# Performance work log

Measured on AMD Instinct MI355X. Metric: run time of the kernel, lower is better.

## Reference

```python
import jax, jax.numpy as jnp
import numpy as np

# SparseSAKEEnergyModel: 6-layer sparse SAKE GNN (hidden=64, heads=4, update=False)
# followed by per-graph segment_sum and a Dense(64)->silu->Dense(1) head.
N_NODES = 10000
N_EDGES = 100000
F_IN = 16           # raw node feature dim (embedded to H by embedding_in)
H = 64              # hidden_features
HEADS = 4           # SAKE default n_heads
COEF = H * HEADS    # n_coefficients = 256
DEPTH = 6
RBF = 50            # ExpNormalSmearing num_rbf
CUT = 5.0           # ExpNormalSmearing cutoff_upper (alpha = 5/(5-0) = 1)
NUM_SEGMENTS = 100


def setup_inputs() -> dict:
    key = jax.random.key(0)
    ks = jax.random.split(key, 20)

    def dn(k, *shape):
        # Dense kernel init ~ lecun-normal-ish: std = 1/sqrt(fan_in); fan_in = shape[-2]
        return jax.random.normal(k, shape, jnp.float32) * np.float32(1.0 / np.sqrt(shape[-2]))

    start = float(np.exp(-CUT))
    rbf_means = jnp.broadcast_to(jnp.linspace(start, 1.0, RBF).astype(jnp.float32)[None], (DEPTH, RBF))
    rbf_betas = jnp.full((DEPTH, RBF), float(((2.0 / RBF) * (1.0 - start)) ** -2), jnp.float32)

    z = lambda *s: jnp.zeros(s, jnp.float32)
    return dict(
        i=jax.random.normal(ks[0], (N_NODES, F_IN), jnp.float32),
        x=jax.random.normal(ks[1], (N_NODES, 3), jnp.float32),
        emb_in_w=dn(ks[2], F_IN, H), emb_in_b=z(H),
        edge_in_w=dn(ks[3], DEPTH, 2 * H, RBF), edge_in_b=z(DEPTH, RBF),
        rbf_means=rbf_means, rbf_betas=rbf_betas,
        edge_out_w1=dn(ks[4], DEPTH, 2 * H + RBF + 1, H), edge_out_b1=z(DEPTH, H),
        edge_out_w2=dn(ks[5], DEPTH, H, H), edge_out_b2=z(DEPTH, H),
        sem_w=dn(ks[6], DEPTH, H, HEADS), sem_b=z(DEPTH, HEADS),
        xmix_w=dn(ks[7], DEPTH, COEF, COEF),
        pn_w1=dn(ks[8], DEPTH, COEF, H), pn_b1=z(DEPTH, H),
        pn_w2=dn(ks[9], DEPTH, H, H), pn_b2=z(DEPTH, H),
        node_w1=dn(ks[10], DEPTH, H + COEF + H, H), node_b1=z(DEPTH, H),
        node_w2=dn(ks[11], DEPTH, H, H), node_b2=z(DEPTH, H),
        emb_out_w1=dn(ks[12], H, H), emb_out_b1=z(H),
        emb_out_w2=dn(ks[13], H, H), emb_out_b2=z(H),
        head_w1=dn(ks[14], H, H), head_b1=z(H),
        head_w2=dn(ks[15], H, 1), head_b2=z(1),
        edges=jax.random.randint(ks[16], (N_EDGES, 2), 0, N_NODES, jnp.int32),
        graph_segments=jnp.sort(jax.random.randint(ks[17], (N_NODES,), 0, NUM_SEGMENTS, jnp.int32)),
    )


def _segment_softmax(logits, seg, num_segments):
    m = jax.ops.segment_max(logits, seg, num_segments)
    e = jnp.exp(logits - m[seg])
    s = jax.ops.segment_sum(e, seg, num_segments)
    return e / s[seg]


def _forward(i, x, emb_in_w, emb_in_b, edge_in_w, edge_in_b, rbf_means, rbf_betas,
             edge_out_w1, edge_out_b1, edge_out_w2, edge_out_b2, sem_w, sem_b, xmix_w,
             pn_w1, pn_b1, pn_w2, pn_b2, node_w1, node_b1, node_w2, node_b2,
             emb_out_w1, emb_out_b1, emb_out_w2, emb_out_b2,
             head_w1, head_b1, head_w2, head_b2, edges, graph_segments):
    N = x.shape[0]
    dst, src = edges[:, 0], edges[:, 1]
    x_minus_xt = x[dst] - x[src]                               # (E,3)
    d = jnp.sqrt((x_minus_xt ** 2).sum(-1, keepdims=True) + 1e-10)  # (E,1)
    dirs = x_minus_xt / (d + 1e-5)                             # normalized edge directions
    rbf_base = jnp.exp(-d)                                     # ExpNormalSmearing, alpha=1, lower=0

    h = i @ emb_in_w + emb_in_b                                # embedding_in -> (N,H)
    for l in range(DEPTH):
        # --- edge model: ContinuousFilterConvolutionWithConcatenation ---
        hc = jnp.concatenate([h[dst], h[src]], -1)             # (E,2H)
        hm = hc @ edge_in_w[l] + edge_in_b[l]                  # (E,RBF)
        rbf = jnp.exp(-rbf_betas[l] * (rbf_base - rbf_means[l]) ** 2)
        he = jnp.concatenate([hc, rbf * hm, d], -1)
        he = jax.nn.silu(he @ edge_out_w1[l] + edge_out_b1[l]) @ edge_out_w2[l] + edge_out_b2[l]  # (E,H)
        # --- combined (semantic * euclidean) attention, segment-softmax over dst ---
        att_s = _segment_softmax(jax.nn.celu(he @ sem_w[l] + sem_b[l], alpha=2.0), dst, N)  # (E,HEADS)
        att_e = _segment_softmax(-d, dst, N)                   # (E,1)
        att = att_e * att_s
        att = att / jax.ops.segment_sum(att, dst, N)[dst]
        hea = (he[:, :, None] * att[:, None, :]).reshape(-1, COEF)  # (E, H*HEADS)
        # --- spatial attention ---
        coef = jnp.tanh(hea @ xmix_w[l])                       # (E,COEF)
        csum = jax.ops.segment_sum(coef[:, :, None] * dirs[:, None, :], dst, N)  # (N,COEF,3)
        cnorm = (csum ** 2).sum(-1)                            # (N,COEF)
        h_comb = jax.nn.silu(jax.nn.silu(cnorm @ pn_w1[l] + pn_b1[l]) @ pn_w2[l] + pn_b2[l])
        # --- aggregate + node update (residual) ---
        h_agg = jax.ops.segment_sum(hea, dst, N)               # (N,COEF)
        upd = jnp.concatenate([h, h_agg, h_comb], -1)
        upd = jax.nn.silu(jax.nn.silu(upd @ node_w1[l] + node_b1[l]) @ node_w2[l] + node_b2[l])
        h = h + upd
    h = jax.nn.silu(h @ emb_out_w1 + emb_out_b1) @ emb_out_w2 + emb_out_b2  # embedding_out
    y = jax.ops.segment_sum(h, graph_segments, NUM_SEGMENTS)   # per-graph readout (G,H)
    return jax.nn.silu(y @ head_w1 + head_b1) @ head_w2 + head_b2  # (G,1)


def reference(i, x, emb_in_w, emb_in_b, edge_in_w, edge_in_b, rbf_means, rbf_betas,
              edge_out_w1, edge_out_b1, edge_out_w2, edge_out_b2, sem_w, sem_b, xmix_w,
              pn_w1, pn_b1, pn_w2, pn_b2, node_w1, node_b1, node_w2, node_b2,
              emb_out_w1, emb_out_b1, emb_out_w2, emb_out_b2,
              head_w1, head_b1, head_w2, head_b2, edges, graph_segments):
    return _forward(i, x, emb_in_w, emb_in_b, edge_in_w, edge_in_b, rbf_means, rbf_betas,
                    edge_out_w1, edge_out_b1, edge_out_w2, edge_out_b2, sem_w, sem_b, xmix_w,
                    pn_w1, pn_b1, pn_w2, pn_b2, node_w1, node_b1, node_w2, node_b2,
                    emb_out_w1, emb_out_b1, emb_out_w2, emb_out_b2,
                    head_w1, head_b1, head_w2, head_b2, edges, graph_segments)
```

## Files before the change

### kernel.cpp

```cpp
#include <hip/hip_runtime.h>
#include <hip/hip_bf16.h>

constexpr int EN   = 100000;
constexpr int NN   = 10000;
constexpr int DEPTH = 6;
constexpr int NSEG = 100;
constexpr int LP   = 40;

typedef unsigned short u16;
typedef __bf16 bf16x8 __attribute__((ext_vector_type(8)));
typedef float  f32x4  __attribute__((ext_vector_type(4)));

__device__ inline float wred_max(float v){
#pragma unroll
  for (int o = 32; o > 0; o >>= 1) v = fmaxf(v, __shfl_xor(v, o, 64));
  return v;
}
__device__ inline float wred_sum(float v){
#pragma unroll
  for (int o = 32; o > 0; o >>= 1) v += __shfl_xor(v, o, 64);
  return v;
}
__device__ inline float siluf(float x){ return x / (1.f + __expf(-x)); }
__device__ inline float fast_tanh(float x){
  float e = __expf(2.f * x);
  return 1.f - 2.f / (e + 1.f);
}
__device__ inline u16 f2bf(float x){
  __hip_bfloat16 h = __float2bfloat16(x);
  return *reinterpret_cast<u16*>(&h);
}
__device__ inline float bf2f(u16 u){
  union { float f; unsigned int ui; } v; v.ui = ((unsigned int)u) << 16; return v.f;
}

__global__ __launch_bounds__(256) void count_k(const int* __restrict__ edges,
                                               int* __restrict__ counts){
  int e = blockIdx.x * 256 + threadIdx.x;
  if (e >= EN) return;
  atomicAdd(&counts[edges[2*e]], 1);
}

__global__ __launch_bounds__(256) void scan_k(const int* __restrict__ counts,
                                              int* __restrict__ offs){
  __shared__ int part[256];
  const int CH = (NN + 255) / 256;
  int t = threadIdx.x;
  int s = 0;
  for (int j = 0; j < CH; ++j){ int idx = t*CH + j; if (idx < NN) s += counts[idx]; }
  part[t] = s;
  __syncthreads();
  if (t == 0){
    int run = 0;
    for (int i = 0; i < 256; ++i){ int v = part[i]; part[i] = run; run += v; }
    offs[NN] = run;
  }
  __syncthreads();
  int run = part[t];
  for (int j = 0; j < CH; ++j){
    int idx = t*CH + j;
    if (idx < NN){ offs[idx] = run; run += counts[idx]; }
  }
}

__global__ __launch_bounds__(256) void geoscat_k(const int* __restrict__ edges,
                                                 const float* __restrict__ x,
                                                 const int* __restrict__ offs,
                                                 int* __restrict__ cursor,
                                                 int* __restrict__ edge_s,
                                                 float* __restrict__ dS,
                                                 float* __restrict__ dirsS,
                                                 float* __restrict__ rbfS){
  int e = blockIdx.x * 256 + threadIdx.x;
  if (e >= EN) return;
  int dst = edges[2*e], src = edges[2*e+1];
  float dx = x[dst*3+0] - x[src*3+0];
  float dy = x[dst*3+1] - x[src*3+1];
  float dz = x[dst*3+2] - x[src*3+2];
  float dd = sqrtf(dx*dx + dy*dy + dz*dz + 1e-10f);
  float inv = 1.f / (dd + 1e-5f);
  int pos = offs[dst] + atomicAdd(&cursor[dst], 1);
  edge_s[2*pos]   = dst;
  edge_s[2*pos+1] = src;
  dS[pos]   = dd;
  rbfS[pos] = __expf(-dd);
  dirsS[3*pos+0] = dx*inv; dirsS[3*pos+1] = dy*inv; dirsS[3*pos+2] = dz*inv;
}

__global__ __launch_bounds__(256) void h2b_k(const float* __restrict__ h,
                                             u16* __restrict__ hbf,
                                             u16* __restrict__ node_in){
  int gid = blockIdx.x * 256 + threadIdx.x;
  if (gid >= NN*64) return;
  int n = gid >> 6, ch = gid & 63;
  u16 b = f2bf(h[gid]);
  hbf[gid] = b;
  node_in[(size_t)n*384 + ch] = b;
}

__global__ void convw_k(const float* __restrict__ src, int K, int N, size_t sStride,
                        u16* __restrict__ dst, int Kpad, int Npad, size_t dStride){
  int idx = blockIdx.x * 256 + threadIdx.x;
  if (idx >= Npad*Kpad) return;
  int n = idx / Kpad, k = idx - n*Kpad;
  float v = (k < K && n < N) ? src[blockIdx.y*sStride + (size_t)k*N + n] : 0.f;
  dst[blockIdx.y*dStride + idx] = f2bf(v);
}

__global__ __launch_bounds__(256) void convx_k(const float* __restrict__ xmix,
                                               u16* __restrict__ xr){
  int idx = blockIdx.x * 256 + threadIdx.x;
  int l = blockIdx.y;
  int q  = idx & 63;
  int n  = (idx >> 6) & 255;
  int hd = idx >> 14;
  xr[(size_t)l*65536 + idx] = f2bf(xmix[(size_t)l*65536 + (size_t)(4*q + hd)*256 + n]);
}

__global__ __launch_bounds__(256) void edge_fused_k(
    const int* __restrict__ edge_s,
    const u16* __restrict__ hbf,
    const float* __restrict__ rbfS,
    const float* __restrict__ dS,
    const u16* __restrict__ Winb,
    const float* __restrict__ bin,
    const float* __restrict__ mean,
    const float* __restrict__ beta,
    const u16* __restrict__ W1b,
    const float* __restrict__ b1,
    const u16* __restrict__ W2b,
    const float* __restrict__ b2,
    const float* __restrict__ sw,
    const float* __restrict__ sb,
    u16* __restrict__ he,
    float* __restrict__ logit){
  __shared__ u16 HC[64*132];
  __shared__ u16 WA[64*132];
  __shared__ u16 T2[64*72];
  __shared__ u16 WB[64*72];
  u16* HE1 = WA;
  const int tid = threadIdx.x, lane = tid & 63, wv = tid >> 6;
  const int l15 = lane & 15, kq = (lane >> 4) * 8;
  const int rsub = (lane >> 4) << 2;
  const int e0 = blockIdx.x * 64;

#pragma unroll
  for (int i = 0; i < 4; ++i){
    int idx = tid + i*256;
    int row = idx >> 4, c = idx & 15;
    int e = min(e0 + row, EN - 1);
    int node = (c < 8) ? edge_s[2*e] : edge_s[2*e+1];
    *reinterpret_cast<uint4*>(HC + row*132 + c*8) =
        *reinterpret_cast<const uint4*>(hbf + (size_t)node*64 + (c & 7)*8);
    *reinterpret_cast<uint4*>(WA + row*132 + c*8) =
        *reinterpret_cast<const uint4*>(Winb + row*128 + c*8);
  }
  __syncthreads();

  f32x4 acc[4];
#pragma unroll
  for (int mt = 0; mt < 4; ++mt) acc[mt] = (f32x4){0.f,0.f,0.f,0.f};
#pragma unroll
  for (int kc = 0; kc < 128; kc += 32){
    bf16x8 bf = *reinterpret_cast<const bf16x8*>(WA + (wv*16 + l15)*132 + kc + kq);
#pragma unroll
    for (int mt = 0; mt < 4; ++mt){
      bf16x8 af = *reinterpret_cast<const bf16x8*>(HC + (mt*16 + l15)*132 + kc + kq);
      acc[mt] = __builtin_amdgcn_mfma_f32_16x16x32_bf16(af, bf, acc[mt], 0, 0, 0);
    }
  }
  {
    int n = wv*16 + l15;
    float bi = 0.f, mn = 0.f, bt = 0.f;
    if (n < 50){ bi = bin[n]; mn = mean[n]; bt = beta[n]; }
#pragma unroll
    for (int mt = 0; mt < 4; ++mt){
#pragma unroll
      for (int r = 0; r < 4; ++r){
        int row = mt*16 + rsub + r;
        int e = min(e0 + row, EN - 1);
        float v;
        if (n < 50){ float df = rbfS[e] - mn; v = __expf(-bt*df*df) * (acc[mt][r] + bi); }
        else if (n == 50) v = dS[e];
        else v = 0.f;
        T2[row*72 + n] = f2bf(v);
      }
    }
  }
  __syncthreads();

#pragma unroll
  for (int i = 0; i < 4; ++i){
    int idx = tid + i*256;
    int row = idx >> 4, c = idx & 15;
    *reinterpret_cast<uint4*>(WA + row*132 + c*8) =
        *reinterpret_cast<const uint4*>(W1b + row*192 + c*8);
  }
#pragma unroll
  for (int i = 0; i < 2; ++i){
    int idx = tid + i*256;
    int row = idx >> 3, cc = (idx & 7)*8;
    *reinterpret_cast<uint4*>(WB + row*72 + cc) =
        *reinterpret_cast<const uint4*>(W1b + row*192 + 128 + cc);
  }
  __syncthreads();

#pragma unroll
  for (int mt = 0; mt < 4; ++mt) acc[mt] = (f32x4){0.f,0.f,0.f,0.f};
#pragma unroll
  for (int kc = 0; kc < 128; kc += 32){
    bf16x8 bf = *reinterpret_cast<const bf16x8*>(WA + (wv*16 + l15)*132 + kc + kq);
#pragma unroll
    for (int mt = 0; mt < 4; ++mt){
      bf16x8 af = *reinterpret_cast<const bf16x8*>(HC + (mt*16 + l15)*132 + kc + kq);
      acc[mt] = __builtin_amdgcn_mfma_f32_16x16x32_bf16(af, bf, acc[mt], 0, 0, 0);
    }
  }
#pragma unroll
  for (int kc = 0; kc < 64; kc += 32){
    bf16x8 bf = *reinterpret_cast<const bf16x8*>(WB + (wv*16 + l15)*72 + kc + kq);
#pragma unroll
    for (int mt = 0; mt < 4; ++mt){
      bf16x8 af = *reinterpret_cast<const bf16x8*>(T2 + (mt*16 + l15)*72 + kc + kq);
      acc[mt] = __builtin_amdgcn_mfma_f32_16x16x32_bf16(af, bf, acc[mt], 0, 0, 0);
    }
  }
  __syncthreads();
  {
    int n = wv*16 + l15;
    float bb = b1[n];
#pragma unroll
    for (int mt = 0; mt < 4; ++mt){
#pragma unroll
      for (int r = 0; r < 4; ++r){
        int row = mt*16 + rsub + r;
        HE1[row*72 + n] = f2bf(siluf(acc[mt][r] + bb));
      }
    }
  }

#pragma unroll
  for (int i = 0; i < 2; ++i){
    int idx = tid + i*256;
    int row = idx >> 3, cc = (idx & 7)*8;
    *reinterpret_cast<uint4*>(WB + row*72 + cc) =
        *reinterpret_cast<const uint4*>(W2b + row*64 + cc);
  }
  __syncthreads();

#pragma unroll
  for (int mt = 0; mt < 4; ++mt) acc[mt] = (f32x4){0.f,0.f,0.f,0.f};
#pragma unroll
  for (int kc = 0; kc < 64; kc += 32){
    bf16x8 bf = *reinterpret_cast<const bf16x8*>(WB + (wv*16 + l15)*72 + kc + kq);
#pragma unroll
    for (int mt = 0; mt < 4; ++mt){
      bf16x8 af = *reinterpret_cast<const bf16x8*>(HE1 + (mt*16 + l15)*72 + kc + kq);
      acc[mt] = __builtin_amdgcn_mfma_f32_16x16x32_bf16(af, bf, acc[mt], 0, 0, 0);
    }
  }
  {
    int n = wv*16 + l15;
    float bb = b2[n];
#pragma unroll
    for (int mt = 0; mt < 4; ++mt){
#pragma unroll
      for (int r = 0; r < 4; ++r){
        int row = mt*16 + rsub + r;
        int e = e0 + row;
        u16 hb = f2bf(acc[mt][r] + bb);
        if (e < EN) he[(size_t)e*64 + n] = hb;
        T2[row*72 + n] = hb;
      }
    }
  }
  __syncthreads();

  {
    int er = tid >> 2, hd = tid & 3;
    float a = sb[hd];
#pragma unroll 8
    for (int k = 0; k < 64; ++k)
      a = fmaf(bf2f(T2[er*72 + k]), sw[k*4 + hd], a);
    float v = a > 0.f ? a : 2.f*(__expf(0.5f*a) - 1.f);
    int e = e0 + er;
    if (e < EN) logit[(size_t)e*4 + hd] = v;
  }
}

__global__ __launch_bounds__(256) void xmix_k(const u16* __restrict__ he,
                                              const float* __restrict__ att,
                                              const u16* __restrict__ Xr,
                                              u16* __restrict__ coef){
  __shared__ u16 B_s[128*72];
  const int tid = threadIdx.x, lane = tid & 63, wave = tid >> 6;
  const int l15 = lane & 15, kq = (lane >> 4) * 8;
  const int rsub = (lane >> 4) << 2;
  const int m0 = blockIdx.x * 128;
  const int n0 = blockIdx.y * 128;

  float a32[2][2][8];
  float4 attA[2];
#pragma unroll
  for (int h = 0; h < 2; ++h){
    int m = min(m0 + h*64 + wave*16 + l15, EN - 1);
    attA[h] = *reinterpret_cast<const float4*>(att + (size_t)m*4);
#pragma unroll
    for (int k2 = 0; k2 < 2; ++k2){
      ushort4 u0 = *reinterpret_cast<const ushort4*>(he + (size_t)m*64 + k2*32 + kq);
      ushort4 u1 = *reinterpret_cast<const ushort4*>(he + (size_t)m*64 + k2*32 + kq + 4);
      a32[h][k2][0] = bf2f(u0.x); a32[h][k2][1] = bf2f(u0.y);
      a32[h][k2][2] = bf2f(u0.z); a32[h][k2][3] = bf2f(u0.w);
      a32[h][k2][4] = bf2f(u1.x); a32[h][k2][5] = bf2f(u1.y);
      a32[h][k2][6] = bf2f(u1.z); a32[h][k2][7] = bf2f(u1.w);
    }
  }

  f32x4 acc[2][8];
#pragma unroll
  for (int h = 0; h < 2; ++h)
#pragma unroll
    for (int c = 0; c < 8; ++c) acc[h][c] = (f32x4){0.f,0.f,0.f,0.f};

  const int srow = tid >> 1;
  const int scol = (tid & 1) * 32;

#pragma unroll
  for (int hd = 0; hd < 4; ++hd){
    {
      const u16* src = Xr + ((size_t)hd*256 + n0 + srow)*64 + scol;
      u16* dst = B_s + srow*72 + scol;
      *reinterpret_cast<uint4*>(dst)      = *reinterpret_cast<const uint4*>(src);
      *reinterpret_cast<uint4*>(dst + 8)  = *reinterpret_cast<const uint4*>(src + 8);
      *reinterpret_cast<uint4*>(dst + 16) = *reinterpret_cast<const uint4*>(src + 16);
      *reinterpret_cast<uint4*>(dst + 24) = *reinterpret_cast<const uint4*>(src + 24);
    }
    __syncthreads();
    bf16x8 afs[2][2];
#pragma unroll
    for (int h = 0; h < 2; ++h){
      float a = (hd==0) ? attA[h].x : (hd==1) ? attA[h].y
              : (hd==2) ? attA[h].z : attA[h].w;
#pragma unroll
      for (int k2 = 0; k2 < 2; ++k2){
        u16 o[8];
#pragma unroll
        for (int j = 0; j < 8; ++j) o[j] = f2bf(a32[h][k2][j] * a);
        afs[h][k2] = *reinterpret_cast<bf16x8*>(o);
      }
    }
#pragma unroll
    for (int k2 = 0; k2 < 2; ++k2){
#pragma unroll
      for (int c = 0; c < 8; ++c){
        bf16x8 bf = *reinterpret_cast<const bf16x8*>(B_s + (c*16 + l15)*72 + k2*32 + kq);
        acc[0][c] = __builtin_amdgcn_mfma_f32_16x16x32_bf16(afs[0][k2], bf, acc[0][c], 0, 0, 0);
        acc[1][c] = __builtin_amdgcn_mfma_f32_16x16x32_bf16(afs[1][k2], bf, acc[1][c], 0, 0, 0);
      }
    }
    __syncthreads();
  }

#pragma unroll
  for (int h = 0; h < 2; ++h){
    const int rbase = m0 + h*64 + wave*16 + rsub;
#pragma unroll
    for (int c = 0; c < 8; ++c){
      int n = n0 + c*16 + l15;
#pragma unroll
      for (int r = 0; r < 4; ++r){
        int m = rbase + r;
        if (m < EN) coef[(size_t)m*256 + n] = f2bf(fast_tanh(acc[h][c][r]));
      }
    }
  }
}

template<int MODE>
__global__ __launch_bounds__(256) void mlp2_k(const u16* __restrict__ A, int lda, int K1,
                                              const u16* __restrict__ W1t,
                                              const float* __restrict__ b1,
                                              const u16* __restrict__ W2t,
                                              const float* __restrict__ b2,
                                              int M,
                                              u16* __restrict__ node_in,
                                              const float* __restrict__ hres,
                                              float* __restrict__ hout,
                                              u16* __restrict__ hbf){
  __shared__ u16 A_s[128*LP];
  __shared__ u16 B_s[64*LP];
  __shared__ u16 T_s[128*72];
  __shared__ u16 W2_s[64*72];
  const int tid = threadIdx.x, lane = tid & 63, wave = tid >> 6;
  const int m0 = blockIdx.x * 128;
  const int l15 = lane & 15, kq = (lane >> 4)*8;
  const int rsub = (lane >> 4) << 2;
#pragma unroll
  for (int i = 0; i < 2; ++i){
    int idx = tid + i*256;
    int row = idx >> 3, cc = (idx & 7)*8;
    *reinterpret_cast<uint4*>(W2_s + row*72 + cc) =
        *reinterpret_cast<const uint4*>(W2t + row*64 + cc);
  }
  const int srow = tid >> 1, skh = (tid & 1)*16;
  const int arow = min(m0 + srow, M - 1);
  const u16* aptr = A + (size_t)arow*lda + skh;
  const int brow = tid >> 2, bcol = (tid & 3)*8;

  f32x4 acc0[4], acc1[4];
#pragma unroll
  for (int c = 0; c < 4; ++c){ acc0[c] = (f32x4){0,0,0,0}; acc1[c] = (f32x4){0,0,0,0}; }

  for (int kc = 0; kc < K1; kc += 32){
    *reinterpret_cast<uint4*>(A_s + srow*LP + skh)     = *reinterpret_cast<const uint4*>(aptr + kc);
    *reinterpret_cast<uint4*>(A_s + srow*LP + skh + 8) = *reinterpret_cast<const uint4*>(aptr + kc + 8);
    *reinterpret_cast<uint4*>(B_s + brow*LP + bcol) =
        *reinterpret_cast<const uint4*>(W1t + (size_t)brow*K1 + kc + bcol);
    __syncthreads();
    bf16x8 af0 = *reinterpret_cast<const bf16x8*>(A_s + (wave*16 + l15)*LP + kq);
    bf16x8 af1 = *reinterpret_cast<const bf16x8*>(A_s + (64 + wave*16 + l15)*LP + kq);
#pragma unroll
    for (int c = 0; c < 4; ++c){
      bf16x8 bf = *reinterpret_cast<const bf16x8*>(B_s + (c*16 + l15)*LP + kq);
      acc0[c] = __builtin_amdgcn_mfma_f32_16x16x32_bf16(af0, bf, acc0[c], 0, 0, 0);
      acc1[c] = __builtin_amdgcn_mfma_f32_16x16x32_bf16(af1, bf, acc1[c], 0, 0, 0);
    }
    __syncthreads();
  }
#pragma unroll
  for (int h = 0; h < 2; ++h){
#pragma unroll
    for (int c = 0; c < 4; ++c){
      int n = c*16 + l15;
      float bb = b1[n];
#pragma unroll
      for (int r = 0; r < 4; ++r){
        int rowloc = h*64 + wave*16 + rsub + r;
        float a = (h == 0) ? acc0[c][r] : acc1[c][r];
        T_s[rowloc*72 + n] = f2bf(siluf(a + bb));
      }
    }
  }
  __syncthreads();
#pragma unroll
  for (int c = 0; c < 4; ++c){ acc0[c] = (f32x4){0,0,0,0}; acc1[c] = (f32x4){0,0,0,0}; }
#pragma unroll
  for (int kc = 0; kc < 64; kc += 32){
    bf16x8 af0 = *reinterpret_cast<const bf16x8*>(T_s + (wave*16 + l15)*72 + kc + kq);
    bf16x8 af1 = *reinterpret_cast<const bf16x8*>(T_s + (64 + wave*16 + l15)*72 + kc + kq);
#pragma unroll
    for (int c = 0; c < 4; ++c){
      bf16x8 bf = *reinterpret_cast<const bf16x8*>(W2_s + (c*16 + l15)*72 + kc + kq);
      acc0[c] = __builtin_amdgcn_mfma_f32_16x16x32_bf16(af0, bf, acc0[c], 0, 0, 0);
      acc1[c] = __builtin_amdgcn_mfma_f32_16x16x32_bf16(af1, bf, acc1[c], 0, 0, 0);
    }
  }
#pragma unroll
  for (int h = 0; h < 2; ++h){
#pragma unroll
    for (int c = 0; c < 4; ++c){
      int n = c*16 + l15;
      float bb = b2[n];
#pragma unroll
      for (int r = 0; r < 4; ++r){
        int m = m0 + h*64 + wave*16 + rsub + r;
        if (m >= M) continue;
        float a = (h == 0) ? acc0[c][r] : acc1[c][r];
        float v = siluf(a + bb);
        if (MODE == 0){
          node_in[(size_t)m*384 + 320 + n] = f2bf(v);
        } else {
          float hn = hres[(size_t)m*64 + n] + v;
          hout[(size_t)m*64 + n] = hn;
          u16 bbf = f2bf(hn);
          hbf[(size_t)m*64 + n] = bbf;
          node_in[(size_t)m*384 + n] = bbf;
        }
      }
    }
  }
}

template<int EPI>
__global__ __launch_bounds__(256) void gemm_k(const float* __restrict__ A, int lda,
                                              const float* __restrict__ W, int ldw,
                                              const float* __restrict__ bias,
                                              float* __restrict__ out, int ldo, int ocol,
                                              int M, int N, int K){
  __shared__ float w_s[128*64];
  const int tid  = threadIdx.x;
  const int nl   = tid & 63;
  const int rg   = tid >> 6;
  const int col0 = blockIdx.y * 64;
  const int m0   = blockIdx.x * 16 + rg * 4;
  float acc[4] = {0.f, 0.f, 0.f, 0.f};
  const float* ar[4];
#pragma unroll
  for (int r = 0; r < 4; ++r){
    int mr = min(m0 + r, M - 1);
    ar[r] = A + (size_t)mr * lda;
  }
  for (int kc = 0; kc < K; kc += 128){
    int kn = min(128, K - kc);
    for (int idx = tid; idx < 128*64; idx += 256){
      int kk = idx >> 6, nn = idx & 63;
      int gn = col0 + nn;
      w_s[idx] = (kk < kn && gn < N) ? W[(size_t)(kc+kk)*ldw + gn] : 0.f;
    }
    __syncthreads();
    for (int k = 0; k < kn; ++k){
      float wv = w_s[k*64 + nl];
#pragma unroll
      for (int r = 0; r < 4; ++r) acc[r] = fmaf(ar[r][kc + k], wv, acc[r]);
    }
    __syncthreads();
  }
  int n = col0 + nl;
  if (n >= N) return;
  float b = bias ? bias[n] : 0.f;
#pragma unroll
  for (int r = 0; r < 4; ++r){
    int m = m0 + r;
    if (m >= M) break;
    float a = acc[r] + b;
    out[(size_t)m*ldo + ocol + n] = (EPI == 1) ? siluf(a) : a;
  }
}

__global__ __launch_bounds__(256) void att_k(const int* __restrict__ offs,
                                             const float* __restrict__ dS,
                                             const float* __restrict__ logit,
                                             float* __restrict__ att){
  int lane = threadIdx.x & 63;
  int node = (blockIdx.x * 256 + threadIdx.x) >> 6;
  if (node >= NN) return;
  int s0 = offs[node];
  int cnt = offs[node+1] - s0;
  if (cnt <= 0) return;
  const float NEG = -1e30f;
  if (cnt <= 64){
    bool act = lane < cnt;
    int p = s0 + (act ? lane : 0);
    float dd = dS[p];
    float4 lg = *reinterpret_cast<const float4*>(logit + 4*(size_t)p);
    float me  = wred_max(act ? -dd  : NEG);
    float ms0 = wred_max(act ? lg.x : NEG);
    float ms1 = wred_max(act ? lg.y : NEG);
    float ms2 = wred_max(act ? lg.z : NEG);
    float ms3 = wred_max(act ? lg.w : NEG);
    float ee  = act ? __expf(-dd - me)  : 0.f;
    float v0  = act ? __expf(lg.x - ms0) : 0.f;
    float v1  = act ? __expf(lg.y - ms1) : 0.f;
    float v2  = act ? __expf(lg.z - ms2) : 0.f;
    float v3  = act ? __expf(lg.w - ms3) : 0.f;
    float ise = 1.f / wred_sum(ee);
    float is0 = 1.f / wred_sum(v0);
    float is1 = 1.f / wred_sum(v1);
    float is2 = 1.f / wred_sum(v2);
    float is3 = 1.f / wred_sum(v3);
    float ae = ee * ise;
    float a0 = ae * v0 * is0, a1 = ae * v1 * is1;
    float a2 = ae * v2 * is2, a3 = ae * v3 * is3;
    float iz0 = 1.f / wred_sum(a0), iz1 = 1.f / wred_sum(a1);
    float iz2 = 1.f / wred_sum(a2), iz3 = 1.f / wred_sum(a3);
    if (act){
      float4 o; o.x = a0*iz0; o.y = a1*iz1; o.z = a2*iz2; o.w = a3*iz3;
      *reinterpret_cast<float4*>(att + 4*(size_t)p) = o;
    }
    return;
  }
  float me = NEG, ms0 = NEG, ms1 = NEG, ms2 = NEG, ms3 = NEG;
  for (int j = lane; j < cnt; j += 64){
    int p = s0 + j;
    float dd = dS[p];
    me = fmaxf(me, -dd);
    float4 lg = *reinterpret_cast<const float4*>(logit + 4*(size_t)p);
    ms0 = fmaxf(ms0, lg.x); ms1 = fmaxf(ms1, lg.y);
    ms2 = fmaxf(ms2, lg.z); ms3 = fmaxf(ms3, lg.w);
  }
  me = wred_max(me); ms0 = wred_max(ms0); ms1 = wred_max(ms1);
  ms2 = wred_max(ms2); ms3 = wred_max(ms3);
  float se = 0.f, ss0 = 0.f, ss1 = 0.f, ss2 = 0.f, ss3 = 0.f;
  for (int j = lane; j < cnt; j += 64){
    int p = s0 + j;
    float dd = dS[p];
    float4 lg = *reinterpret_cast<const float4*>(logit + 4*(size_t)p);
    se  += __expf(-dd - me);
    ss0 += __expf(lg.x - ms0); ss1 += __expf(lg.y - ms1);
    ss2 += __expf(lg.z - ms2); ss3 += __expf(lg.w - ms3);
  }
  se = wred_sum(se); ss0 = wred_sum(ss0); ss1 = wred_sum(ss1);
  ss2 = wred_sum(ss2); ss3 = wred_sum(ss3);
  float ise = 1.f/se, is0 = 1.f/ss0, is1 = 1.f/ss1, is2 = 1.f/ss2, is3 = 1.f/ss3;
  float z0 = 0.f, z1 = 0.f, z2 = 0.f, z3 = 0.f;
  for (int j = lane; j < cnt; j += 64){
    int p = s0 + j;
    float dd = dS[p];
    float4 lg = *reinterpret_cast<const float4*>(logit + 4*(size_t)p);
    float ae = __expf(-dd - me) * ise;
    z0 += ae * __expf(lg.x - ms0) * is0;
    z1 += ae * __expf(lg.y - ms1) * is1;
    z2 += ae * __expf(lg.z - ms2) * is2;
    z3 += ae * __expf(lg.w - ms3) * is3;
  }
  z0 = wred_sum(z0); z1 = wred_sum(z1); z2 = wred_sum(z2); z3 = wred_sum(z3);
  float iz0 = 1.f/z0, iz1 = 1.f/z1, iz2 = 1.f/z2, iz3 = 1.f/z3;
  for (int j = lane; j < cnt; j += 64){
    int p = s0 + j;
    float dd = dS[p];
    float4 lg = *reinterpret_cast<const float4*>(logit + 4*(size_t)p);
    float ae = __expf(-dd - me) * ise;
    float4 o;
    o.x = ae * __expf(lg.x - ms0) * is0 * iz0;
    o.y = ae * __expf(lg.y - ms1) * is1 * iz1;
    o.z = ae * __expf(lg.z - ms2) * is2 * iz2;
    o.w = ae * __expf(lg.w - ms3) * is3 * iz3;
    *reinterpret_cast<float4*>(att + 4*(size_t)p) = o;
  }
}

__global__ __launch_bounds__(256) void agg_k(const int* __restrict__ offs,
                                             const u16* __restrict__ coef,
                                             const u16* __restrict__ he,
                                             const float* __restrict__ att,
                                             const float* __restrict__ dirsS,
                                             u16* __restrict__ cnorm,
                                             u16* __restrict__ node_in){
  int node = blockIdx.x;
  int c = threadIdx.x;
  int s0 = offs[node], s1 = offs[node+1];
  int q = c >> 2, hd = c & 3;
  float cs0 = 0.f, cs1 = 0.f, cs2 = 0.f, ha = 0.f;
  for (int p = s0; p < s1; ++p){
    float co = bf2f(coef[(size_t)p*256 + c]);
    float hv = bf2f(he[(size_t)p*64 + q]);
    float av = att[(size_t)p*4 + hd];
    float d0 = dirsS[3*(size_t)p], d1 = dirsS[3*(size_t)p+1], d2 = dirsS[3*(size_t)p+2];
    cs0 = fmaf(co, d0, cs0); cs1 = fmaf(co, d1, cs1); cs2 = fmaf(co, d2, cs2);
    ha = fmaf(hv, av, ha);
  }
  cnorm[(size_t)node*256 + c] = f2bf(cs0*cs0 + cs1*cs1 + cs2*cs2);
  node_in[(size_t)node*384 + 64 + c] = f2bf(ha);
}

__global__ __launch_bounds__(256) void segy_k(const float* __restrict__ hf,
                                              const int* __restrict__ seg,
                                              float* __restrict__ y){
  int gid = blockIdx.x * 256 + threadIdx.x;
  if (gid >= NN*64) return;
  int n = gid >> 6, ch = gid & 63;
  atomicAdd(&y[seg[n]*64 + ch], hf[gid]);
}

__global__ void headf_k(const float* __restrict__ t2,
                        const float* __restrict__ w2,
                        const float* __restrict__ b2,
                        float* __restrict__ out){
  int s = threadIdx.x;
  if (s >= NSEG) return;
  float acc = b2[0];
  for (int k = 0; k < 64; ++k) acc = fmaf(t2[s*64 + k], w2[k], acc);
  out[s] = acc;
}

extern "C" void kernel_launch(void* const* d_in, const int* in_sizes, int n_in,
                              void* d_out, int out_size, void* d_ws, size_t ws_size,
                              hipStream_t stream) {
  (void)in_sizes; (void)n_in; (void)out_size; (void)ws_size;
  const float* in_i       = (const float*)d_in[0];
  const float* in_x       = (const float*)d_in[1];
  const float* emb_in_w   = (const float*)d_in[2];
  const float* emb_in_b   = (const float*)d_in[3];
  const float* edge_in_w  = (const float*)d_in[4];
  const float* edge_in_b  = (const float*)d_in[5];
  const float* rbf_means  = (const float*)d_in[6];
  const float* rbf_betas  = (const float*)d_in[7];
  const float* edge_o_w1  = (const float*)d_in[8];
  const float* edge_o_b1  = (const float*)d_in[9];
  const float* edge_o_w2  = (const float*)d_in[10];
  const float* edge_o_b2  = (const float*)d_in[11];
  const float* sem_w      = (const float*)d_in[12];
  const float* sem_b      = (const float*)d_in[13];
  const float* xmix_w     = (const float*)d_in[14];
  const float* pn_w1      = (const float*)d_in[15];
  const float* pn_b1      = (const float*)d_in[16];
  const float* pn_w2      = (const float*)d_in[17];
  const float* pn_b2      = (const float*)d_in[18];
  const float* node_w1    = (const float*)d_in[19];
  const float* node_b1    = (const float*)d_in[20];
  const float* node_w2    = (const float*)d_in[21];
  const float* node_b2    = (const float*)d_in[22];
  const float* emb_o_w1   = (const float*)d_in[23];
  const float* emb_o_b1   = (const float*)d_in[24];
  const float* emb_o_w2   = (const float*)d_in[25];
  const float* emb_o_b2   = (const float*)d_in[26];
  const float* head_w1    = (const float*)d_in[27];
  const float* head_b1    = (const float*)d_in[28];
  const float* head_w2    = (const float*)d_in[29];
  const float* head_b2    = (const float*)d_in[30];
  const int*   edges      = (const int*)d_in[31];
  const int*   segs       = (const int*)d_in[32];
  float* out = (float*)d_out;

  char* base = (char*)d_ws;
  size_t off = 0;
  auto alloc = [&](size_t bytes) -> void* {
    void* p = base + off;
    off += (bytes + 255) & ~(size_t)255;
    return p;
  };
  float* dS     = (float*)alloc((size_t)EN*4);
  float* dirsS  = (float*)alloc((size_t)EN*3*4);
  float* rbfS   = (float*)alloc((size_t)EN*4);
  int*   edge_s = (int*)alloc((size_t)EN*2*4);
  float* hA     = (float*)alloc((size_t)NN*64*4);
  float* hB     = (float*)alloc((size_t)NN*64*4);
  u16*   he     = (u16*)alloc((size_t)EN*64*2);
  u16*   coef   = (u16*)alloc((size_t)EN*256*2);
  float* logit  = (float*)alloc((size_t)EN*4*4);
  float* att    = (float*)alloc((size_t)EN*4*4);
  u16*   hbf    = (u16*)alloc((size_t)NN*64*2);
  u16*   node_in= (u16*)alloc((size_t)NN*384*2);
  u16*   cnorm  = (u16*)alloc((size_t)NN*256*2);
  float* y      = (float*)alloc((size_t)NSEG*64*4);
  float* t2     = (float*)alloc((size_t)NSEG*64*4);
  u16* winb  = (u16*)alloc((size_t)DEPTH*64*128*2);
  u16* w1b   = (u16*)alloc((size_t)DEPTH*64*192*2);
  u16* w2b   = (u16*)alloc((size_t)DEPTH*64*64*2);
  u16* xr    = (u16*)alloc((size_t)DEPTH*4*256*64*2);
  u16* pw1b  = (u16*)alloc((size_t)DEPTH*64*256*2);
  u16* pw2b  = (u16*)alloc((size_t)DEPTH*64*64*2);
  u16* nw1b  = (u16*)alloc((size_t)DEPTH*64*384*2);
  u16* nw2b  = (u16*)alloc((size_t)DEPTH*64*64*2);
  int* counts   = (int*)alloc((size_t)NN*4);
  int* cursor   = (int*)alloc((size_t)NN*4);
  int* offs     = (int*)alloc((size_t)(NN+1)*4);
  float* t_node = (float*)coef;

  hipMemsetAsync(counts, 0, (size_t)NN*4, stream);
  hipMemsetAsync(cursor, 0, (size_t)NN*4, stream);
  hipMemsetAsync(y, 0, (size_t)NSEG*64*4, stream);

  count_k<<<(EN+255)/256, 256, 0, stream>>>(edges, counts);
  scan_k<<<1, 256, 0, stream>>>(counts, offs);
  geoscat_k<<<(EN+255)/256, 256, 0, stream>>>(edges, in_x, offs, cursor,
                                              edge_s, dS, dirsS, rbfS);

  convw_k<<<dim3(32,  DEPTH), 256, 0, stream>>>(edge_in_w, 128, 50, (size_t)128*50, winb, 128, 64, (size_t)64*128);
  convw_k<<<dim3(48,  DEPTH), 256, 0, stream>>>(edge_o_w1, 179, 64, (size_t)179*64, w1b,  192, 64, (size_t)64*192);
  convw_k<<<dim3(16,  DEPTH), 256, 0, stream>>>(edge_o_w2,  64, 64, (size_t)64*64,  w2b,   64, 64, (size_t)64*64);
  convx_k<<<dim3(256, DEPTH), 256, 0, stream>>>(xmix_w, xr);
  convw_k<<<dim3(64,  DEPTH), 256, 0, stream>>>(pn_w1,     256, 64, (size_t)256*64, pw1b, 256, 64, (size_t)64*256);
  convw_k<<<dim3(16,  DEPTH), 256, 0, stream>>>(pn_w2,      64, 64, (size_t)64*64,  pw2b,  64, 64, (size_t)64*64);
  convw_k<<<dim3(96,  DEPTH), 256, 0, stream>>>(node_w1,   384, 64, (size_t)384*64, nw1b, 384, 64, (size_t)64*384);
  convw_k<<<dim3(16,  DEPTH), 256, 0, stream>>>(node_w2,    64, 64, (size_t)64*64,  nw2b,  64, 64, (size_t)64*64);

  gemm_k<0><<<dim3((NN+15)/16, 1), 256, 0, stream>>>(
      in_i, 16, emb_in_w, 64, emb_in_b, hA, 64, 0, NN, 64, 16);
  h2b_k<<<(NN*64)/256, 256, 0, stream>>>(hA, hbf, node_in);

  const int EB  = (EN + 63) / 64;
  const int EB2 = (EN + 127) / 128;
  const int NB2 = (NN + 127) / 128;

  float* hcur = hA;
  float* hnext = hB;
  for (int l = 0; l < DEPTH; ++l){
    const float* bin  = edge_in_b + (size_t)l*50;
    const float* mean = rbf_means + (size_t)l*50;
    const float* beta = rbf_betas + (size_t)l*50;
    const float* b1   = edge_o_b1 + (size_t)l*64;
    const float* b2   = edge_o_b2 + (size_t)l*64;
    const float* sw   = sem_w + (size_t)l*64*4;
    const float* sb   = sem_b + (size_t)l*4;
    const float* pb1  = pn_b1 + (size_t)l*64;
    const float* pb2  = pn_b2 + (size_t)l*64;
    const float* nb1  = node_b1 + (size_t)l*64;
    const float* nb2  = node_b2 + (size_t)l*64;
    const u16* Winb = winb + (size_t)l*64*128;
    const u16* W1b  = w1b  + (size_t)l*64*192;
    const u16* W2b  = w2b  + (size_t)l*64*64;
    const u16* Xrl  = xr   + (size_t)l*65536;
    const u16* P1b  = pw1b + (size_t)l*64*256;
    const u16* P2b  = pw2b + (size_t)l*64*64;
    const u16* N1b  = nw1b + (size_t)l*64*384;
    const u16* N2b  = nw2b + (size_t)l*64*64;

    edge_fused_k<<<EB, 256, 0, stream>>>(edge_s, hbf, rbfS, dS,
                                         Winb, bin, mean, beta,
                                         W1b, b1, W2b, b2, sw, sb,
                                         he, logit);
    att_k<<<(NN+3)/4, 256, 0, stream>>>(offs, dS, logit, att);
    xmix_k<<<dim3(EB2, 2), 256, 0, stream>>>(he, att, Xrl, coef);
    agg_k<<<NN, 256, 0, stream>>>(offs, coef, he, att, dirsS, cnorm, node_in);
    mlp2_k<0><<<NB2, 256, 0, stream>>>(cnorm, 256, 256, P1b, pb1, P2b, pb2, NN,
                                       node_in, nullptr, nullptr, nullptr);
    mlp2_k<1><<<NB2, 256, 0, stream>>>(node_in, 384, 384, N1b, nb1, N2b, nb2, NN,
                                       node_in, hcur, hnext, hbf);
    float* tmp = hcur; hcur = hnext; hnext = tmp;
  }

  gemm_k<1><<<dim3((NN+15)/16, 1), 256, 0, stream>>>(
      hcur, 64, emb_o_w1, 64, emb_o_b1, t_node, 64, 0, NN, 64, 64);
  gemm_k<0><<<dim3((NN+15)/16, 1), 256, 0, stream>>>(
      t_node, 64, emb_o_w2, 64, emb_o_b2, hnext, 64, 0, NN, 64, 64);
  segy_k<<<(NN*64)/256, 256, 0, stream>>>(hnext, segs, y);
  gemm_k<1><<<dim3((NSEG+15)/16, 1), 256, 0, stream>>>(
      y, 64, head_w1, 64, head_b1, t2, 64, 0, NSEG, 64, 64);
  headf_k<<<1, 128, 0, stream>>>(t2, head_w2, head_b2, out);
}
```

Before: 1.071 ms.

## Fuse node MLPs per layer, read edge weights from global, bf16 MFMA embedding-out

The edge kernel now reads weight fragments directly from global memory (L1/L2 cached) instead of staging them in LDS. This drops several weight-staging passes and barriers and frees LDS for higher occupancy. The two per-layer node MLP kernels are fused into one nodeblock kernel that keeps the post-norm MLP output in LDS rather than writing it to node_in and re-reading it. The fp32 embedding-out GEMMs are replaced by a single bf16 MFMA two-layer MLP kernel, which adds bf16 rounding of the final hidden state.

```diff
diff --git a/kernel.cpp b/kernel.cpp
--- a/kernel.cpp
+++ b/kernel.cpp
@@ -32,6 +32,9 @@
 }
 __device__ inline float bf2f(u16 u){
   union { float f; unsigned int ui; } v; v.ui = ((unsigned int)u) << 16; return v.f;
+}
+__device__ inline bf16x8 ldg_bf8(const u16* p){
+  return *reinterpret_cast<const bf16x8*>(p);
 }
 
 __global__ __launch_bounds__(256) void count_k(const int* __restrict__ edges,
@@ -135,14 +138,13 @@
     u16* __restrict__ he,
     float* __restrict__ logit){
   __shared__ u16 HC[64*132];
-  __shared__ u16 WA[64*132];
   __shared__ u16 T2[64*72];
-  __shared__ u16 WB[64*72];
-  u16* HE1 = WA;
+  __shared__ u16 HE1[64*72];
   const int tid = threadIdx.x, lane = tid & 63, wv = tid >> 6;
   const int l15 = lane & 15, kq = (lane >> 4) * 8;
   const int rsub = (lane >> 4) << 2;
   const int e0 = blockIdx.x * 64;
+  const int nw = wv*16 + l15;
 
 #pragma unroll
   for (int i = 0; i < 4; ++i){
@@ -152,8 +154,6 @@
     int node = (c < 8) ? edge_s[2*e] : edge_s[2*e+1];
     *reinterpret_cast<uint4*>(HC + row*132 + c*8) =
         *reinterpret_cast<const uint4*>(hbf + (size_t)node*64 + (c & 7)*8);
-    *reinterpret_cast<uint4*>(WA + row*132 + c*8) =
-        *reinterpret_cast<const uint4*>(Winb + row*128 + c*8);
   }
   __syncthreads();
 
@@ -162,7 +162,7 @@
   for (int mt = 0; mt < 4; ++mt) acc[mt] = (f32x4){0.f,0.f,0.f,0.f};
 #pragma unroll
   for (int kc = 0; kc < 128; kc += 32){
-    bf16x8 bf = *reinterpret_cast<const bf16x8*>(WA + (wv*16 + l15)*132 + kc + kq);
+    bf16x8 bf = ldg_bf8(Winb + nw*128 + kc + kq);
 #pragma unroll
     for (int mt = 0; mt < 4; ++mt){
       bf16x8 af = *reinterpret_cast<const bf16x8*>(HC + (mt*16 + l15)*132 + kc + kq);
@@ -170,9 +170,8 @@
     }
   }
   {
-    int n = wv*16 + l15;
     float bi = 0.f, mn = 0.f, bt = 0.f;
-    if (n < 50){ bi = bin[n]; mn = mean[n]; bt = beta[n]; }
+    if (nw < 50){ bi = bin[nw]; mn = mean[nw]; bt = beta[nw]; }
 #pragma unroll
     for (int mt = 0; mt < 4; ++mt){
 #pragma unroll
@@ -180,36 +179,20 @@
         int row = mt*16 + rsub + r;
         int e = min(e0 + row, EN - 1);
         float v;
-        if (n < 50){ float df = rbfS[e] - mn; v = __expf(-bt*df*df) * (acc[mt][r] + bi); }
-        else if (n == 50) v = dS[e];
+        if (nw < 50){ float df = rbfS[e] - mn; v = __expf(-bt*df*df) * (acc[mt][r] + bi); }
+        else if (nw == 50) v = dS[e];
         else v = 0.f;
-        T2[row*72 + n] = f2bf(v);
+        T2[row*72 + nw] = f2bf(v);
       }
     }
   }
   __syncthreads();
 
 #pragma unroll
-  for (int i = 0; i < 4; ++i){
-    int idx = tid + i*256;
-    int row = idx >> 4, c = idx & 15;
-    *reinterpret_cast<uint4*>(WA + row*132 + c*8) =
-        *reinterpret_cast<const uint4*>(W1b + row*192 + c*8);
-  }
-#pragma unroll
-  for (int i = 0; i < 2; ++i){
-    int idx = tid + i*256;
-    int row = idx >> 3, cc = (idx & 7)*8;
-    *reinterpret_cast<uint4*>(WB + row*72 + cc) =
-        *reinterpret_cast<const uint4*>(W1b + row*192 + 128 + cc);
-  }
-  __syncthreads();
-
-#pragma unroll
   for (int mt = 0; mt < 4; ++mt) acc[mt] = (f32x4){0.f,0.f,0.f,0.f};
 #pragma unroll
   for (int kc = 0; kc < 128; kc += 32){
-    bf16x8 bf = *reinterpret_cast<const bf16x8*>(WA + (wv*16 + l15)*132 + kc + kq);
+    bf16x8 bf = ldg_bf8(W1b + nw*192 + kc + kq);
 #pragma unroll
     for (int mt = 0; mt < 4; ++mt){
       bf16x8 af = *reinterpret_cast<const bf16x8*>(HC + (mt*16 + l15)*132 + kc + kq);
@@ -217,34 +200,24 @@
     }
   }
 #pragma unroll
-  for (int kc = 0; kc < 64; kc += 32){
-    bf16x8 bf = *reinterpret_cast<const bf16x8*>(WB + (wv*16 + l15)*72 + kc + kq);
+  for (int kc = 128; kc < 192; kc += 32){
+    bf16x8 bf = ldg_bf8(W1b + nw*192 + kc + kq);
 #pragma unroll
     for (int mt = 0; mt < 4; ++mt){
-      bf16x8 af = *reinterpret_cast<const bf16x8*>(T2 + (mt*16 + l15)*72 + kc + kq);
+      bf16x8 af = *reinterpret_cast<const bf16x8*>(T2 + (mt*16 + l15)*72 + (kc-128) + kq);
       acc[mt] = __builtin_amdgcn_mfma_f32_16x16x32_bf16(af, bf, acc[mt], 0, 0, 0);
     }
   }
-  __syncthreads();
   {
-    int n = wv*16 + l15;
-    float bb = b1[n];
+    float bb = b1[nw];
 #pragma unroll
     for (int mt = 0; mt < 4; ++mt){
 #pragma unroll
       for (int r = 0; r < 4; ++r){
         int row = mt*16 + rsub + r;
-        HE1[row*72 + n] = f2bf(siluf(acc[mt][r] + bb));
-      }
-    }
-  }
-
-#pragma unroll
-  for (int i = 0; i < 2; ++i){
-    int idx = tid + i*256;
-    int row = idx >> 3, cc = (idx & 7)*8;
-    *reinterpret_cast<uint4*>(WB + row*72 + cc) =
-        *reinterpret_cast<const uint4*>(W2b + row*64 + cc);
+        HE1[row*72 + nw] = f2bf(siluf(acc[mt][r] + bb));
+      }
+    }
   }
   __syncthreads();
 
@@ -252,7 +225,7 @@
   for (int mt = 0; mt < 4; ++mt) acc[mt] = (f32x4){0.f,0.f,0.f,0.f};
 #pragma unroll
   for (int kc = 0; kc < 64; kc += 32){
-    bf16x8 bf = *reinterpret_cast<const bf16x8*>(WB + (wv*16 + l15)*72 + kc + kq);
+    bf16x8 bf = ldg_bf8(W2b + nw*64 + kc + kq);
 #pragma unroll
     for (int mt = 0; mt < 4; ++mt){
       bf16x8 af = *reinterpret_cast<const bf16x8*>(HE1 + (mt*16 + l15)*72 + kc + kq);
@@ -260,8 +233,7 @@
     }
   }
   {
-    int n = wv*16 + l15;
-    float bb = b2[n];
+    float bb = b2[nw];
 #pragma unroll
     for (int mt = 0; mt < 4; ++mt){
 #pragma unroll
@@ -269,8 +241,8 @@
         int row = mt*16 + rsub + r;
         int e = e0 + row;
         u16 hb = f2bf(acc[mt][r] + bb);
-        if (e < EN) he[(size_t)e*64 + n] = hb;
-        T2[row*72 + n] = hb;
+        if (e < EN) he[(size_t)e*64 + nw] = hb;
+        T2[row*72 + nw] = hb;
       }
     }
   }
@@ -376,17 +348,195 @@
   }
 }
 
-template<int MODE>
-__global__ __launch_bounds__(256) void mlp2_k(const u16* __restrict__ A, int lda, int K1,
-                                              const u16* __restrict__ W1t,
-                                              const float* __restrict__ b1,
-                                              const u16* __restrict__ W2t,
-                                              const float* __restrict__ b2,
-                                              int M,
-                                              u16* __restrict__ node_in,
-                                              const float* __restrict__ hres,
-                                              float* __restrict__ hout,
-                                              u16* __restrict__ hbf){
+__global__ __launch_bounds__(256) void nodeblock_k(
+    const u16* __restrict__ cnorm,
+    const u16* __restrict__ P1t, const float* __restrict__ pb1,
+    const u16* __restrict__ P2t, const float* __restrict__ pb2,
+    const u16* __restrict__ node_in,
+    const u16* __restrict__ N1t, const float* __restrict__ nb1,
+    const u16* __restrict__ N2t, const float* __restrict__ nb2,
+    const float* __restrict__ hres,
+    float* __restrict__ hout,
+    u16* __restrict__ hbf,
+    u16* __restrict__ node_io){
+  __shared__ u16 A_s[128*LP];
+  __shared__ u16 B_s[64*LP];
+  __shared__ u16 T_s[128*72];
+  __shared__ u16 W2_s[64*72];
+  __shared__ u16 HCm[128*72];
+  const int tid = threadIdx.x, lane = tid & 63, wave = tid >> 6;
+  const int m0 = blockIdx.x * 128;
+  const int l15 = lane & 15, kq = (lane >> 4)*8;
+  const int rsub = (lane >> 4) << 2;
+  const int srow = tid >> 1, skh = (tid & 1)*16;
+  const int arow = min(m0 + srow, NN - 1);
+  const u16* aptr1 = cnorm + (size_t)arow*256 + skh;
+  const u16* aptr2 = node_in + (size_t)arow*384 + skh;
+  const int brow = tid >> 2, bcol = (tid & 3)*8;
+
+#pragma unroll
+  for (int i = 0; i < 2; ++i){
+    int idx = tid + i*256;
+    int row = idx >> 3, cc = (idx & 7)*8;
+    *reinterpret_cast<uint4*>(W2_s + row*72 + cc) =
+        *reinterpret_cast<const uint4*>(P2t + row*64 + cc);
+  }
+
+  f32x4 acc0[4], acc1[4];
+#pragma unroll
+  for (int c = 0; c < 4; ++c){ acc0[c] = (f32x4){0,0,0,0}; acc1[c] = (f32x4){0,0,0,0}; }
+
+  for (int kc = 0; kc < 256; kc += 32){
+    *reinterpret_cast<uint4*>(A_s + srow*LP + skh)     = *reinterpret_cast<const uint4*>(aptr1 + kc);
+    *reinterpret_cast<uint4*>(A_s + srow*LP + skh + 8) = *reinterpret_cast<const uint4*>(aptr1 + kc + 8);
+    *reinterpret_cast<uint4*>(B_s + brow*LP + bcol) =
+        *reinterpret_cast<const uint4*>(P1t + (size_t)brow*256 + kc + bcol);
+    __syncthreads();
+    bf16x8 af0 = *reinterpret_cast<const bf16x8*>(A_s + (wave*16 + l15)*LP + kq);
+    bf16x8 af1 = *reinterpret_cast<const bf16x8*>(A_s + (64 + wave*16 + l15)*LP + kq);
+#pragma unroll
+    for (int c = 0; c < 4; ++c){
+      bf16x8 bf = *reinterpret_cast<const bf16x8*>(B_s + (c*16 + l15)*LP + kq);
+      acc0[c] = __builtin_amdgcn_mfma_f32_16x16x32_bf16(af0, bf, acc0[c], 0, 0, 0);
+      acc1[c] = __builtin_amdgcn_mfma_f32_16x16x32_bf16(af1, bf, acc1[c], 0, 0, 0);
+    }
+    __syncthreads();
+  }
+#pragma unroll
+  for (int h = 0; h < 2; ++h){
+#pragma unroll
+    for (int c = 0; c < 4; ++c){
+      int n = c*16 + l15;
+      float bb = pb1[n];
+#pragma unroll
+      for (int r = 0; r < 4; ++r){
+        int rowloc = h*64 + wave*16 + rsub + r;
+        float a = (h == 0) ? acc0[c][r] : acc1[c][r];
+        T_s[rowloc*72 + n] = f2bf(siluf(a + bb));
+      }
+    }
+  }
+  __syncthreads();
+#pragma unroll
+  for (int c = 0; c < 4; ++c){ acc0[c] = (f32x4){0,0,0,0}; acc1[c] = (f32x4){0,0,0,0}; }
+#pragma unroll
+  for (int kc = 0; kc < 64; kc += 32){
+    bf16x8 af0 = *reinterpret_cast<const bf16x8*>(T_s + (wave*16 + l15)*72 + kc + kq);
+    bf16x8 af1 = *reinterpret_cast<const bf16x8*>(T_s + (64 + wave*16 + l15)*72 + kc + kq);
+#pragma unroll
+    for (int c = 0; c < 4; ++c){
+      bf16x8 bf = *reinterpret_cast<const bf16x8*>(W2_s + (c*16 + l15)*72 + kc + kq);
+      acc0[c] = __builtin_amdgcn_mfma_f32_16x16x32_bf16(af0, bf, acc0[c], 0, 0, 0);
+      acc1[c] = __builtin_amdgcn_mfma_f32_16x16x32_bf16(af1, bf, acc1[c], 0, 0, 0);
+    }
+  }
+#pragma unroll
+  for (int h = 0; h < 2; ++h){
+#pragma unroll
+    for (int c = 0; c < 4; ++c){
+      int n = c*16 + l15;
+      float bb = pb2[n];
+#pragma unroll
+      for (int r = 0; r < 4; ++r){
+        int rowloc = h*64 + wave*16 + rsub + r;
+        float a = (h == 0) ? acc0[c][r] : acc1[c][r];
+        HCm[rowloc*72 + n] = f2bf(siluf(a + bb));
+      }
+    }
+  }
+  __syncthreads();
+
+#pragma unroll
+  for (int c = 0; c < 4; ++c){ acc0[c] = (f32x4){0,0,0,0}; acc1[c] = (f32x4){0,0,0,0}; }
+  for (int kc = 0; kc < 320; kc += 32){
+    *reinterpret_cast<uint4*>(A_s + srow*LP + skh)     = *reinterpret_cast<const uint4*>(aptr2 + kc);
+    *reinterpret_cast<uint4*>(A_s + srow*LP + skh + 8) = *reinterpret_cast<const uint4*>(aptr2 + kc + 8);
+    *reinterpret_cast<uint4*>(B_s + brow*LP + bcol) =
+        *reinterpret_cast<const uint4*>(N1t + (size_t)brow*384 + kc + bcol);
+    __syncthreads();
+    bf16x8 af0 = *reinterpret_cast<const bf16x8*>(A_s + (wave*16 + l15)*LP + kq);
+    bf16x8 af1 = *reinterpret_cast<const bf16x8*>(A_s + (64 + wave*16 + l15)*LP + kq);
+#pragma unroll
+    for (int c = 0; c < 4; ++c){
+      bf16x8 bf = *reinterpret_cast<const bf16x8*>(B_s + (c*16 + l15)*LP + kq);
+      acc0[c] = __builtin_amdgcn_mfma_f32_16x16x32_bf16(af0, bf, acc0[c], 0, 0, 0);
+      acc1[c] = __builtin_amdgcn_mfma_f32_16x16x32_bf16(af1, bf, acc1[c], 0, 0, 0);
+    }
+    __syncthreads();
+  }
+#pragma unroll
+  for (int kc = 320; kc < 384; kc += 32){
+    bf16x8 af0 = *reinterpret_cast<const bf16x8*>(HCm + (wave*16 + l15)*72 + (kc-320) + kq);
+    bf16x8 af1 = *reinterpret_cast<const bf16x8*>(HCm + (64 + wave*16 + l15)*72 + (kc-320) + kq);
+#pragma unroll
+    for (int c = 0; c < 4; ++c){
+      bf16x8 bf = ldg_bf8(N1t + (size_t)(c*16 + l15)*384 + kc + kq);
+      acc0[c] = __builtin_amdgcn_mfma_f32_16x16x32_bf16(af0, bf, acc0[c], 0, 0, 0);
+      acc1[c] = __builtin_amdgcn_mfma_f32_16x16x32_bf16(af1, bf, acc1[c], 0, 0, 0);
+    }
+  }
+#pragma unroll
+  for (int h = 0; h < 2; ++h){
+#pragma unroll
+    for (int c = 0; c < 4; ++c){
+      int n = c*16 + l15;
+      float bb = nb1[n];
+#pragma unroll
+      for (int r = 0; r < 4; ++r){
+        int rowloc = h*64 + wave*16 + rsub + r;
+        float a = (h == 0) ? acc0[c][r] : acc1[c][r];
+        T_s[rowloc*72 + n] = f2bf(siluf(a + bb));
+      }
+    }
+  }
+#pragma unroll
+  for (int i = 0; i < 2; ++i){
+    int idx = tid + i*256;
+    int row = idx >> 3, cc = (idx & 7)*8;
+    *reinterpret_cast<uint4*>(W2_s + row*72 + cc) =
+        *reinterpret_cast<const uint4*>(N2t + row*64 + cc);
+  }
+  __syncthreads();
+#pragma unroll
+  for (int c = 0; c < 4; ++c){ acc0[c] = (f32x4){0,0,0,0}; acc1[c] = (f32x4){0,0,0,0}; }
+#pragma unroll
+  for (int kc = 0; kc < 64; kc += 32){
+    bf16x8 af0 = *reinterpret_cast<const bf16x8*>(T_s + (wave*16 + l15)*72 + kc + kq);
+    bf16x8 af1 = *reinterpret_cast<const bf16x8*>(T_s + (64 + wave*16 + l15)*72 + kc + kq);
+#pragma unroll
+    for (int c = 0; c < 4; ++c){
+      bf16x8 bf = *reinterpret_cast<const bf16x8*>(W2_s + (c*16 + l15)*72 + kc + kq);
+      acc0[c] = __builtin_amdgcn_mfma_f32_16x16x32_bf16(af0, bf, acc0[c], 0, 0, 0);
+      acc1[c] = __builtin_amdgcn_mfma_f32_16x16x32_bf16(af1, bf, acc1[c], 0, 0, 0);
+    }
+  }
+#pragma unroll
+  for (int h = 0; h < 2; ++h){
+#pragma unroll
+    for (int c = 0; c < 4; ++c){
+      int n = c*16 + l15;
+      float bb = nb2[n];
+#pragma unroll
+      for (int r = 0; r < 4; ++r){
+        int m = m0 + h*64 + wave*16 + rsub + r;
+        if (m >= NN) continue;
+        float a = (h == 0) ? acc0[c][r] : acc1[c][r];
+        float hn = hres[(size_t)m*64 + n] + siluf(a + bb);
+        hout[(size_t)m*64 + n] = hn;
+        u16 bbf = f2bf(hn);
+        hbf[(size_t)m*64 + n] = bbf;
+        node_io[(size_t)m*384 + n] = bbf;
+      }
+    }
+  }
+}
+
+__global__ __launch_bounds__(256) void mlp2_head_k(const u16* __restrict__ A,
+                                                   const u16* __restrict__ W1t,
+                                                   const float* __restrict__ b1,
+                                                   const u16* __restrict__ W2t,
+                                                   const float* __restrict__ b2,
+                                                   float* __restrict__ outf){
   __shared__ u16 A_s[128*LP];
   __shared__ u16 B_s[64*LP];
   __shared__ u16 T_s[128*72];
@@ -403,19 +553,18 @@
         *reinterpret_cast<const uint4*>(W2t + row*64 + cc);
   }
   const int srow = tid >> 1, skh = (tid & 1)*16;
-  const int arow = min(m0 + srow, M - 1);
-  const u16* aptr = A + (size_t)arow*lda + skh;
+  const int arow = min(m0 + srow, NN - 1);
+  const u16* aptr = A + (size_t)arow*64 + skh;
+
+  f32x4 acc0[4], acc1[4];
+#pragma unroll
+  for (int c = 0; c < 4; ++c){ acc0[c] = (f32x4){0,0,0,0}; acc1[c] = (f32x4){0,0,0,0}; }
   const int brow = tid >> 2, bcol = (tid & 3)*8;
-
-  f32x4 acc0[4], acc1[4];
-#pragma unroll
-  for (int c = 0; c < 4; ++c){ acc0[c] = (f32x4){0,0,0,0}; acc1[c] = (f32x4){0,0,0,0}; }
-
-  for (int kc = 0; kc < K1; kc += 32){
+  for (int kc = 0; kc < 64; kc += 32){
     *reinterpret_cast<uint4*>(A_s + srow*LP + skh)     = *reinterpret_cast<const uint4*>(aptr + kc);
     *reinterpret_cast<uint4*>(A_s + srow*LP + skh + 8) = *reinterpret_cast<const uint4*>(aptr + kc + 8);
     *reinterpret_cast<uint4*>(B_s + brow*LP + bcol) =
-        *reinterpret_cast<const uint4*>(W1t + (size_t)brow*K1 + kc + bcol);
+        *reinterpret_cast<const uint4*>(W1t + (size_t)brow*64 + kc + bcol);
     __syncthreads();
     bf16x8 af0 = *reinterpret_cast<const bf16x8*>(A_s + (wave*16 + l15)*LP + kq);
     bf16x8 af1 = *reinterpret_cast<const bf16x8*>(A_s + (64 + wave*16 + l15)*LP + kq);
@@ -464,18 +613,9 @@
 #pragma unroll
       for (int r = 0; r < 4; ++r){
         int m = m0 + h*64 + wave*16 + rsub + r;
-        if (m >= M) continue;
+        if (m >= NN) continue;
         float a = (h == 0) ? acc0[c][r] : acc1[c][r];
-        float v = siluf(a + bb);
-        if (MODE == 0){
-          node_in[(size_t)m*384 + 320 + n] = f2bf(v);
-        } else {
-          float hn = hres[(size_t)m*64 + n] + v;
-          hout[(size_t)m*64 + n] = hn;
-          u16 bbf = f2bf(hn);
-          hbf[(size_t)m*64 + n] = bbf;
-          node_in[(size_t)m*384 + n] = bbf;
-        }
+        outf[(size_t)m*64 + n] = a + bb;
       }
     }
   }
@@ -732,10 +872,11 @@
   u16* pw2b  = (u16*)alloc((size_t)DEPTH*64*64*2);
   u16* nw1b  = (u16*)alloc((size_t)DEPTH*64*384*2);
   u16* nw2b  = (u16*)alloc((size_t)DEPTH*64*64*2);
+  u16* eo1b  = (u16*)alloc((size_t)64*64*2);
+  u16* eo2b  = (u16*)alloc((size_t)64*64*2);
   int* counts   = (int*)alloc((size_t)NN*4);
   int* cursor   = (int*)alloc((size_t)NN*4);
   int* offs     = (int*)alloc((size_t)(NN+1)*4);
-  float* t_node = (float*)coef;
 
   hipMemsetAsync(counts, 0, (size_t)NN*4, stream);
   hipMemsetAsync(cursor, 0, (size_t)NN*4, stream);
@@ -754,6 +895,8 @@
   convw_k<<<dim3(16,  DEPTH), 256, 0, stream>>>(pn_w2,      64, 64, (size_t)64*64,  pw2b,  64, 64, (size_t)64*64);
   convw_k<<<dim3(96,  DEPTH), 256, 0, stream>>>(node_w1,   384, 64, (size_t)384*64, nw1b, 384, 64, (size_t)64*384);
   convw_k<<<dim3(16,  DEPTH), 256, 0, stream>>>(node_w2,    64, 64, (size_t)64*64,  nw2b,  64, 64, (size_t)64*64);
+  convw_k<<<dim3(16,  1),     256, 0, stream>>>(emb_o_w1,   64, 64, (size_t)64*64,  eo1b,  64, 64, (size_t)64*64);
+  convw_k<<<dim3(16,  1),     256, 0, stream>>>(emb_o_w2,   64, 64, (size_t)64*64,  eo2b,  64, 64, (size_t)64*64);
 
   gemm_k<0><<<dim3((NN+15)/16, 1), 256, 0, stream>>>(
       in_i, 16, emb_in_w, 64, emb_in_b, hA, 64, 0, NN, 64, 16);
@@ -793,17 +936,13 @@
     att_k<<<(NN+3)/4, 256, 0, stream>>>(offs, dS, logit, att);
     xmix_k<<<dim3(EB2, 2), 256, 0, stream>>>(he, att, Xrl, coef);
     agg_k<<<NN, 256, 0, stream>>>(offs, coef, he, att, dirsS, cnorm, node_in);
-    mlp2_k<0><<<NB2, 256, 0, stream>>>(cnorm, 256, 256, P1b, pb1, P2b, pb2, NN,
-                                       node_in, nullptr, nullptr, nullptr);
-    mlp2_k<1><<<NB2, 256, 0, stream>>>(node_in, 384, 384, N1b, nb1, N2b, nb2, NN,
-                                       node_in, hcur, hnext, hbf);
+    nodeblock_k<<<NB2, 256, 0, stream>>>(cnorm, P1b, pb1, P2b, pb2,
+                                         node_in, N1b, nb1, N2b, nb2,
+                                         hcur, hnext, hbf, node_in);
     float* tmp = hcur; hcur = hnext; hnext = tmp;
   }
 
-  gemm_k<1><<<dim3((NN+15)/16, 1), 256, 0, stream>>>(
-      hcur, 64, emb_o_w1, 64, emb_o_b1, t_node, 64, 0, NN, 64, 64);
-  gemm_k<0><<<dim3((NN+15)/16, 1), 256, 0, stream>>>(
-      t_node, 64, emb_o_w2, 64, emb_o_b2, hnext, 64, 0, NN, 64, 64);
+  mlp2_head_k<<<NB2, 256, 0, stream>>>(hbf, eo1b, emb_o_b1, eo2b, emb_o_b2, hnext);
   segy_k<<<(NN*64)/256, 256, 0, stream>>>(hnext, segs, y);
   gemm_k<1><<<dim3((NSEG+15)/16, 1), 256, 0, stream>>>(
       y, 64, head_w1, 64, head_b1, t2, 64, 0, NSEG, 64, 64);
```

Measured after the change: 1.009 ms. 5.8% less time.
